# Kernel optimization log

Measured on AMD Instinct MI355X. Metric: run time of the kernel, lower is better.

## Reference

```python
import jax, jax.numpy as jnp
import numpy as np

N_DATA = 500000
EMB = 256
K = 4096
BS = 64
T = 0.07
M = 0.5


def _l2norm(x, axis=-1, eps=1e-12):
    return x / jnp.maximum(jnp.linalg.norm(x, axis=axis, keepdims=True), eps)


def setup_inputs() -> dict:
    key = jax.random.key(0)
    k1, k2, k3, k4, k5, k6 = jax.random.split(key, 6)
    vis_feat = jax.random.normal(k1, (BS, EMB), dtype=jnp.float32)
    text_feat = jax.random.normal(k2, (BS, EMB), dtype=jnp.float32)
    # memory banks: original inits uniform in [-stdv, stdv]; randn scaled works the same numerically
    stdv = 1.0 / np.sqrt(EMB / 3)
    vis_memory = jax.random.uniform(k3, (N_DATA, EMB), dtype=jnp.float32, minval=-stdv, maxval=stdv)
    text_memory = jax.random.uniform(k4, (N_DATA, EMB), dtype=jnp.float32, minval=-stdv, maxval=stdv)
    idx = jax.random.randint(k5, (BS,), 0, N_DATA, dtype=jnp.int32)
    slct_idx = jax.random.randint(k6, (BS, K + 1), 0, N_DATA, dtype=jnp.int32)
    # column 0 holds the positive index, as in slct_idx.select(1,0).copy_(idx)
    slct_idx = slct_idx.at[:, 0].set(idx)
    return {
        "vis_feat": vis_feat,
        "text_feat": text_feat,
        "vis_memory": vis_memory,
        "text_memory": text_memory,
        "slct_idx": slct_idx,
        "idx": idx,
    }


def reference(vis_feat, text_feat, vis_memory, text_memory, slct_idx, idx):
    # embeddings are L2-normalized before use (nn.functional.normalize(dim=1))
    vn = _l2norm(vis_feat)   # [bs, D]
    tn = _l2norm(text_feat)  # [bs, D]

    # gather K+1 negatives/positive from memory banks (detached in original)
    tf = jax.lax.stop_gradient(text_memory[slct_idx])  # [bs, K+1, D]
    vf = jax.lax.stop_gradient(vis_memory[slct_idx])   # [bs, K+1, D]

    # batched dot products + exp(./T) (bmm with [bs, D, 1])
    vis_out = jnp.exp(jnp.einsum("bkd,bd->bk", tf, vn) / T)   # [bs, K+1]
    text_out = jnp.exp(jnp.einsum("bkd,bd->bk", vf, tn) / T)  # [bs, K+1]

    # NCE normalization constants, set on first pass: Z = mean * N_data
    Z_v = jax.lax.stop_gradient(jnp.mean(vis_out)) * N_DATA
    Z_t = jax.lax.stop_gradient(jnp.mean(text_out)) * N_DATA
    vis_out = vis_out / Z_v
    text_out = text_out / Z_t

    # EMA memory update + renormalize + scatter (no_grad in original)
    vis_pos = vis_memory[idx] * M + jax.lax.stop_gradient(vn) * (1.0 - M)
    text_pos = text_memory[idx] * M + jax.lax.stop_gradient(tn) * (1.0 - M)
    new_vis_memory = vis_memory.at[idx].set(_l2norm(vis_pos))
    new_text_memory = text_memory.at[idx].set(_l2norm(text_pos))

    return vis_out, text_out, new_vis_memory, new_text_memory
```

## Files before the change

kernel.cpp:

```cpp
#include <hip/hip_runtime.h>

#define NDATA 500000
#define EMB   256
#define BS    64
#define KP1   4097
#define NPAIR (BS * KP1)
#define INV_T (1.0f / 0.07f)

#define SCAN_EPB 2048
#define NB_SCAN  ((NDATA + SCAN_EPB - 1) / SCAN_EPB)
#define RPW      32
#define NWAVES   (NDATA / RPW)
#define NBLKF    ((NWAVES + 3) / 4)
#define SSC_BLKS ((NPAIR + 255) / 256)
#define SCALE_BLKS ((2 * NPAIR + 255) / 256)
#define NBY      17

typedef float    f32x4 __attribute__((ext_vector_type(4)));
typedef unsigned u32x4 __attribute__((ext_vector_type(4)));

__global__ __launch_bounds__(256) void norm_hist_kernel(
    const float* __restrict__ vis_feat, const float* __restrict__ text_feat,
    float* __restrict__ vn, float* __restrict__ tn,
    const int* __restrict__ slct, unsigned* __restrict__ counts,
    unsigned* __restrict__ old) {
  int bid = blockIdx.x;
  if (bid < 128) {
    int b = bid & 63;
    bool is_vis = bid < 64;
    const float* src = (is_vis ? vis_feat : text_feat) + b * EMB;
    float* dst = (is_vis ? vn : tn) + b * EMB;
    int t = threadIdx.x;
    float x = src[t];
    float s = x * x;
    for (int off = 32; off > 0; off >>= 1) s += __shfl_down(s, off, 64);
    __shared__ float red[4];
    if ((t & 63) == 0) red[t >> 6] = s;
    __syncthreads();
    float norm = sqrtf(red[0] + red[1] + red[2] + red[3]);
    dst[t] = x / fmaxf(norm, 1e-12f);
  } else {
    int i = (bid - 128) * 256 + threadIdx.x;
    if (i < NPAIR) {
      int r = slct[i];
      old[i] = atomicAdd(&counts[r], 1u);
    }
  }
}

__global__ __launch_bounds__(256) void scan1_kernel(
    const unsigned* __restrict__ counts, unsigned* __restrict__ start,
    unsigned* __restrict__ bsum) {
  int t = threadIdx.x;
  int base = blockIdx.x * SCAN_EPB + t * 8;
  unsigned v[8];
  unsigned tsum = 0;
#pragma unroll
  for (int j = 0; j < 8; ++j) {
    int i = base + j;
    unsigned c = (i < NDATA) ? counts[i] : 0u;
    v[j] = tsum;
    tsum += c;
  }
  unsigned x = tsum;
  for (int d = 1; d < 64; d <<= 1) {
    unsigned y = __shfl_up(x, d, 64);
    if ((t & 63) >= d) x += y;
  }
  __shared__ unsigned wsum[4];
  if ((t & 63) == 63) wsum[t >> 6] = x;
  __syncthreads();
  unsigned woff = 0;
  for (int wv = 0; wv < (t >> 6); ++wv) woff += wsum[wv];
  unsigned ex = woff + x - tsum;
#pragma unroll
  for (int j = 0; j < 8; ++j) {
    int i = base + j;
    if (i < NDATA) start[i] = ex + v[j];
  }
  if (t == 255) bsum[blockIdx.x] = woff + x;
}

__global__ __launch_bounds__(256) void scan2_kernel(unsigned* __restrict__ bsum) {
  int t = threadIdx.x;
  unsigned v = (t < NB_SCAN) ? bsum[t] : 0u;
  unsigned x = v;
  for (int d = 1; d < 64; d <<= 1) {
    unsigned y = __shfl_up(x, d, 64);
    if ((t & 63) >= d) x += y;
  }
  __shared__ unsigned wsum[4];
  if ((t & 63) == 63) wsum[t >> 6] = x;
  __syncthreads();
  unsigned woff = 0;
  for (int wv = 0; wv < (t >> 6); ++wv) woff += wsum[wv];
  unsigned ex = woff + x - v;
  if (t < NB_SCAN) bsum[t] = ex;
}

__global__ __launch_bounds__(256) void scatter_kernel(
    const int* __restrict__ slct, const unsigned* __restrict__ start,
    const unsigned* __restrict__ bsum, const unsigned* __restrict__ old,
    unsigned* __restrict__ pairs) {
  int i = blockIdx.x * 256 + threadIdx.x;
  if (i < NPAIR) {
    int r = slct[i];
    unsigned pos = start[r] + bsum[r >> 11] + old[i];
    int b = i / KP1;
    int kk = i - b * KP1;
    pairs[pos] = ((unsigned)b << 13) | (unsigned)kk;
  }
}

#define LOADC(R, rb)                                                          \
  { _Pragma("unroll") for (int j = 0; j < 8; ++j)                             \
      R[j] = __builtin_nontemporal_load(&s4[(size_t)((rb) + j) * 64 + lane]); }

#define STOREC(R, rb)                                                         \
  { _Pragma("unroll") for (int j = 0; j < 8; ++j)                             \
      __builtin_nontemporal_store(R[j], &d4[(size_t)((rb) + j) * 64 + lane]); }

#define DOT4(Rj, fv) (Rj.x * fv.x + Rj.y * fv.y + Rj.z * fv.z + Rj.w * fv.w)

#define REFS(R, rb)                                                           \
  { u32x4 c0 = *(const u32x4*)&counts[(rb)];                                  \
    u32x4 c1 = *(const u32x4*)&counts[(rb) + 4];                              \
    u32x4 s0 = *(const u32x4*)&start[(rb)];                                   \
    u32x4 s1 = *(const u32x4*)&start[(rb) + 4];                               \
    unsigned cn[8] = {c0.x, c0.y, c0.z, c0.w, c1.x, c1.y, c1.z, c1.w};        \
    unsigned sn[8] = {s0.x, s0.y, s0.z, s0.w, s1.x, s1.y, s1.z, s1.w};        \
    _Pragma("unroll") for (int j = 0; j < 8; ++j) {                           \
      unsigned n = cn[j];                                                     \
      if (n) {                                                                \
        unsigned gs = sn[j] + bs;                                             \
        unsigned u = 0;                                                       \
        for (; u + 4 <= n; u += 4) {                                          \
          unsigned p0 = pairs[gs + u],     p1 = pairs[gs + u + 1];            \
          unsigned p2 = pairs[gs + u + 2], p3 = pairs[gs + u + 3];            \
          f32x4 f0 = f4[(p0 >> 13) * 64 + lane];                              \
          f32x4 f1 = f4[(p1 >> 13) * 64 + lane];                              \
          f32x4 f2 = f4[(p2 >> 13) * 64 + lane];                              \
          f32x4 f3 = f4[(p3 >> 13) * 64 + lane];                              \
          float d0 = DOT4(R[j], f0), d1 = DOT4(R[j], f1);                     \
          float d2 = DOT4(R[j], f2), d3 = DOT4(R[j], f3);                     \
          for (int off = 32; off > 0; off >>= 1) {                            \
            d0 += __shfl_down(d0, off, 64);                                   \
            d1 += __shfl_down(d1, off, 64);                                   \
            d2 += __shfl_down(d2, off, 64);                                   \
            d3 += __shfl_down(d3, off, 64);                                   \
          }                                                                   \
          if (lane == 0) {                                                    \
            float e0 = __expf(d0 * INV_T), e1 = __expf(d1 * INV_T);           \
            float e2 = __expf(d2 * INV_T), e3 = __expf(d3 * INV_T);           \
            tz[gs + u] = e0; tz[gs + u + 1] = e1;                             \
            tz[gs + u + 2] = e2; tz[gs + u + 3] = e3;                         \
            local += (e0 + e1) + (e2 + e3);                                   \
          }                                                                   \
        }                                                                     \
        for (; u < n; ++u) {                                                  \
          unsigned p = pairs[gs + u];                                         \
          f32x4 fv = f4[(p >> 13) * 64 + lane];                               \
          float d = DOT4(R[j], fv);                                           \
          for (int off = 32; off > 0; off >>= 1) d += __shfl_down(d, off, 64);\
          if (lane == 0) {                                                    \
            float e = __expf(d * INV_T);                                      \
            tz[gs + u] = e;                                                   \
            local += e;                                                       \
          }                                                                   \
        }                                                                     \
      }                                                                       \
    } }

__global__ __launch_bounds__(256) void fused_copy_dot_kernel(
    const float* __restrict__ text_mem, const float* __restrict__ vis_mem,
    float* __restrict__ out_text, float* __restrict__ out_vis,
    const float* __restrict__ vn, const float* __restrict__ tn,
    const unsigned* __restrict__ counts, const unsigned* __restrict__ start,
    const unsigned* __restrict__ bsum, const unsigned* __restrict__ pairs,
    float* __restrict__ tmp0, float* __restrict__ tmp1,
    float* __restrict__ zsum) {
  int z = blockIdx.z;
  const f32x4* s4 = (const f32x4*)(z == 0 ? text_mem : vis_mem);
  f32x4* d4 = (f32x4*)(z == 0 ? out_text : out_vis);
  const f32x4* f4 = (const f32x4*)(z == 0 ? vn : tn);
  float* tz = (z == 0) ? tmp0 : tmp1;

  int t = threadIdx.x, w = t >> 6, lane = t & 63;
  int gw = blockIdx.x * 4 + w;
  float local = 0.f;

  if (gw < NWAVES) {
    int r0 = gw * RPW;
    unsigned bs = bsum[r0 >> 11];
    f32x4 A[8], B[8];
    LOADC(A, r0);
    LOADC(B, r0 + 8);
    STOREC(A, r0);      REFS(A, r0);
    LOADC(A, r0 + 16);
    STOREC(B, r0 + 8);  REFS(B, r0 + 8);
    LOADC(B, r0 + 24);
    STOREC(A, r0 + 16); REFS(A, r0 + 16);
    STOREC(B, r0 + 24); REFS(B, r0 + 24);
  }
  __shared__ float red[4];
  if (lane == 0) red[w] = local;
  __syncthreads();
  if (t == 0) {
    float s = red[0] + red[1] + red[2] + red[3];
    atomicAdd(&zsum[z], s);
  }
}

__global__ __launch_bounds__(256) void scatter_scale_update_kernel(
    const unsigned* __restrict__ pairs,
    const float* __restrict__ tmp0, const float* __restrict__ tmp1,
    float* __restrict__ out, const float* __restrict__ zsum,
    const float* __restrict__ vis_mem, const float* __restrict__ text_mem,
    const float* __restrict__ vn, const float* __restrict__ tn,
    const int* __restrict__ idx,
    float* __restrict__ out_vis, float* __restrict__ out_text) {
  int bid = blockIdx.x;
  if (bid < SSC_BLKS) {
    int pos = bid * 256 + threadIdx.x;
    if (pos < NPAIR) {
      const float c = (float)NDATA / (float)NPAIR;
      unsigned p = pairs[pos];
      int o = (int)(p >> 13) * KP1 + (int)(p & 8191u);
      out[o]         = tmp0[pos] / (zsum[0] * c);
      out[NPAIR + o] = tmp1[pos] / (zsum[1] * c);
    }
  } else {
    int bb = bid - SSC_BLKS;
    int b = bb & 63;
    bool is_vis = bb < 64;
    int row = idx[b];
    for (int b2 = b + 1; b2 < BS; ++b2)
      if (idx[b2] == row) return;
    const float* mem  = (is_vis ? vis_mem : text_mem) + (size_t)row * EMB;
    const float* feat = (is_vis ? vn : tn) + b * EMB;
    float* dst = (is_vis ? out_vis : out_text) + (size_t)row * EMB;
    int t = threadIdx.x;
    float p = mem[t] * 0.5f + feat[t] * 0.5f;
    float s = p * p;
    for (int off = 32; off > 0; off >>= 1) s += __shfl_down(s, off, 64);
    __shared__ float red[4];
    if ((t & 63) == 0) red[t >> 6] = s;
    __syncthreads();
    float norm = sqrtf(red[0] + red[1] + red[2] + red[3]);
    dst[t] = p / fmaxf(norm, 1e-12f);
  }
}

__global__ __launch_bounds__(256) void dot_exp_kernel(
    const float* __restrict__ text_mem, const float* __restrict__ vis_mem,
    const float* __restrict__ vn, const float* __restrict__ tn,
    const int* __restrict__ slct, float* __restrict__ out,
    float* __restrict__ partials) {
  int b = blockIdx.x;
  int z = blockIdx.z;
  const float* mem  = (z == 0) ? text_mem : vis_mem;
  const float* feat = (z == 0) ? vn : tn;
  float* o = out + (size_t)z * NPAIR + (size_t)b * KP1;
  const int* srow = slct + b * KP1;
  __shared__ float4 sf[64];
  int t = threadIdx.x;
  if (t < 64) sf[t] = ((const float4*)(feat + b * EMB))[t];
  __syncthreads();
  int w = t >> 6, lane = t & 63;
  float4 f = sf[lane];
  int kbase = blockIdx.y * 256 + w * 64;
  int kend  = min(kbase + 64, KP1);
  float local = 0.f;
  int k = kbase;
  for (; k + 2 <= kend; k += 2) {
    int r0 = srow[k], r1 = srow[k + 1];
    float4 v0 = ((const float4*)(mem + (size_t)r0 * EMB))[lane];
    float4 v1 = ((const float4*)(mem + (size_t)r1 * EMB))[lane];
    float p0 = v0.x * f.x + v0.y * f.y + v0.z * f.z + v0.w * f.w;
    float p1 = v1.x * f.x + v1.y * f.y + v1.z * f.z + v1.w * f.w;
    for (int off = 32; off > 0; off >>= 1) {
      p0 += __shfl_down(p0, off, 64);
      p1 += __shfl_down(p1, off, 64);
    }
    if (lane == 0) {
      float e0 = __expf(p0 * INV_T);
      float e1 = __expf(p1 * INV_T);
      o[k] = e0; o[k + 1] = e1;
      local += e0 + e1;
    }
  }
  if (k < kend) {
    int r0 = srow[k];
    float4 v0 = ((const float4*)(mem + (size_t)r0 * EMB))[lane];
    float p0 = v0.x * f.x + v0.y * f.y + v0.z * f.z + v0.w * f.w;
    for (int off = 32; off > 0; off >>= 1) p0 += __shfl_down(p0, off, 64);
    if (lane == 0) { float e0 = __expf(p0 * INV_T); o[k] = e0; local += e0; }
  }
  __shared__ float red[4];
  if (lane == 0) red[w] = local;
  __syncthreads();
  if (t == 0)
    partials[((size_t)z * NBY + blockIdx.y) * BS + b] =
        red[0] + red[1] + red[2] + red[3];
}

__global__ __launch_bounds__(256) void reduce_z_kernel(
    const float* __restrict__ partials, float* __restrict__ zsum, int per_z) {
  int z = blockIdx.x;
  const float* p = partials + (size_t)z * per_z;
  float s = 0.f;
  for (int i = threadIdx.x; i < per_z; i += 256) s += p[i];
  for (int off = 32; off > 0; off >>= 1) s += __shfl_down(s, off, 64);
  __shared__ float red[4];
  if ((threadIdx.x & 63) == 0) red[threadIdx.x >> 6] = s;
  __syncthreads();
  if (threadIdx.x == 0) zsum[z] = red[0] + red[1] + red[2] + red[3];
}

__global__ __launch_bounds__(256) void copy2_kernel(
    const float4* __restrict__ src_a, float4* __restrict__ dst_a,
    const float4* __restrict__ src_b, float4* __restrict__ dst_b, long n4) {
  long i = (long)blockIdx.x * blockDim.x + threadIdx.x;
  long stride = (long)gridDim.x * blockDim.x;
  for (; i < 2 * n4; i += stride) {
    if (i < n4) dst_a[i] = src_a[i];
    else        dst_b[i - n4] = src_b[i - n4];
  }
}

__global__ __launch_bounds__(256) void scale_update_kernel(
    float* __restrict__ out, const float* __restrict__ zsum,
    const float* __restrict__ vis_mem, const float* __restrict__ text_mem,
    const float* __restrict__ vn, const float* __restrict__ tn,
    const int* __restrict__ idx,
    float* __restrict__ out_vis, float* __restrict__ out_text) {
  int bid = blockIdx.x;
  if (bid < SCALE_BLKS) {
    int i = bid * 256 + threadIdx.x;
    if (i < 2 * NPAIR) {
      float Z = ((i < NPAIR) ? zsum[0] : zsum[1]) * ((float)NDATA / (float)NPAIR);
      out[i] = out[i] / Z;
    }
  } else {
    int bb = bid - SCALE_BLKS;
    int b = bb & 63;
    bool is_vis = bb < 64;
    int row = idx[b];
    for (int b2 = b + 1; b2 < BS; ++b2)
      if (idx[b2] == row) return;
    const float* mem  = (is_vis ? vis_mem : text_mem) + (size_t)row * EMB;
    const float* feat = (is_vis ? vn : tn) + b * EMB;
    float* dst = (is_vis ? out_vis : out_text) + (size_t)row * EMB;
    int t = threadIdx.x;
    float p = mem[t] * 0.5f + feat[t] * 0.5f;
    float s = p * p;
    for (int off = 32; off > 0; off >>= 1) s += __shfl_down(s, off, 64);
    __shared__ float red[4];
    if ((t & 63) == 0) red[t >> 6] = s;
    __syncthreads();
    float norm = sqrtf(red[0] + red[1] + red[2] + red[3]);
    dst[t] = p / fmaxf(norm, 1e-12f);
  }
}

extern "C" void kernel_launch(void* const* d_in, const int* in_sizes, int n_in,
                              void* d_out, int out_size, void* d_ws, size_t ws_size,
                              hipStream_t stream) {
  const float* vis_feat  = (const float*)d_in[0];
  const float* text_feat = (const float*)d_in[1];
  const float* vis_mem   = (const float*)d_in[2];
  const float* text_mem  = (const float*)d_in[3];
  const int*   slct      = (const int*)d_in[4];
  const int*   idx       = (const int*)d_in[5];

  float* out          = (float*)d_out;
  float* out_vis_mem  = out + (size_t)2 * NPAIR;
  float* out_text_mem = out_vis_mem + (size_t)NDATA * EMB;

  float*    ws     = (float*)d_ws;
  float*    zsum   = ws;
  unsigned* counts = (unsigned*)(zsum + 4);
  unsigned* start  = counts + NDATA;
  unsigned* bsum   = start + NDATA;
  unsigned* old    = bsum + 256;
  unsigned* pairs  = old + NPAIR;
  float*    tmp1   = (float*)(pairs + NPAIR);
  float*    vn     = tmp1 + NPAIR;
  float*    tn     = vn + BS * EMB;
  float*    tmp0   = (float*)old;
  size_t needed = ((size_t)(4 + 2 * NDATA + 256 + 3 * NPAIR) +
                   (size_t)(2 * BS * EMB)) * 4;

  if (ws_size >= needed) {
    hipMemsetAsync(zsum, 0, (4 + NDATA) * sizeof(unsigned), stream);
    norm_hist_kernel<<<128 + (NPAIR + 255) / 256, 256, 0, stream>>>(
        vis_feat, text_feat, vn, tn, slct, counts, old);
    scan1_kernel<<<NB_SCAN, 256, 0, stream>>>(counts, start, bsum);
    scan2_kernel<<<1, 256, 0, stream>>>(bsum);
    scatter_kernel<<<(NPAIR + 255) / 256, 256, 0, stream>>>(slct, start, bsum, old, pairs);

    dim3 gF(NBLKF, 1, 2);
    fused_copy_dot_kernel<<<gF, 256, 0, stream>>>(
        text_mem, vis_mem, out_text_mem, out_vis_mem, vn, tn,
        counts, start, bsum, pairs, tmp0, tmp1, zsum);

    scatter_scale_update_kernel<<<SSC_BLKS + 128, 256, 0, stream>>>(
        pairs, tmp0, tmp1, out, zsum, vis_mem, text_mem, vn, tn, idx,
        out_vis_mem, out_text_mem);
  } else {
    norm_hist_kernel<<<128, 256, 0, stream>>>(
        vis_feat, text_feat, vn, tn, slct, counts, old);
    dim3 gB(BS, NBY, 2);
    dot_exp_kernel<<<gB, 256, 0, stream>>>(text_mem, vis_mem, vn, tn, slct, out,
                                           (float*)old);
    reduce_z_kernel<<<2, 256, 0, stream>>>((float*)old, zsum, NBY * BS);
    const long n4 = (long)NDATA * EMB / 4;
    copy2_kernel<<<8192, 256, 0, stream>>>(
        (const float4*)vis_mem,  (float4*)out_vis_mem,
        (const float4*)text_mem, (float4*)out_text_mem, n4);
    scale_update_kernel<<<SCALE_BLKS + 128, 256, 0, stream>>>(
        out, zsum, vis_mem, text_mem, vn, tn, idx, out_vis_mem, out_text_mem);
  }
}
```

Measured before the change: 421.3 us.

## Fuse block-sum scan into scatter kernel and interleave per-row reference loops

Merges the single-block scan2 kernel into the scatter kernel: every block recomputes the exclusive scan of block sums in shared memory, and block 0 writes the result to a separate bsum2 buffer. This removes one kernel launch and its dependency gap. It also rewrites the per-row reference processing in the fused copy/dot kernel so that the 8 rows of a chunk are handled together, iterating up to the maximum count and issuing up to 8 independent gathers and shuffle reductions per step. The aim is more memory-level parallelism in place of serial per-row loops, at the cost of predicated idle lanes when counts differ and more registers.

```diff
diff --git a/kernel.cpp b/kernel.cpp
--- a/kernel.cpp
+++ b/kernel.cpp
@@ -81,7 +81,12 @@
   if (t == 255) bsum[blockIdx.x] = woff + x;
 }
 
-__global__ __launch_bounds__(256) void scan2_kernel(unsigned* __restrict__ bsum) {
+__global__ __launch_bounds__(256) void scatter2_kernel(
+    const int* __restrict__ slct, const unsigned* __restrict__ start,
+    const unsigned* __restrict__ bsum, const unsigned* __restrict__ old,
+    unsigned* __restrict__ pairs, unsigned* __restrict__ bsum2) {
+  __shared__ unsigned sbs[256];
+  __shared__ unsigned wsum[4];
   int t = threadIdx.x;
   unsigned v = (t < NB_SCAN) ? bsum[t] : 0u;
   unsigned x = v;
@@ -89,23 +94,17 @@
     unsigned y = __shfl_up(x, d, 64);
     if ((t & 63) >= d) x += y;
   }
-  __shared__ unsigned wsum[4];
   if ((t & 63) == 63) wsum[t >> 6] = x;
   __syncthreads();
   unsigned woff = 0;
   for (int wv = 0; wv < (t >> 6); ++wv) woff += wsum[wv];
-  unsigned ex = woff + x - v;
-  if (t < NB_SCAN) bsum[t] = ex;
-}
-
-__global__ __launch_bounds__(256) void scatter_kernel(
-    const int* __restrict__ slct, const unsigned* __restrict__ start,
-    const unsigned* __restrict__ bsum, const unsigned* __restrict__ old,
-    unsigned* __restrict__ pairs) {
-  int i = blockIdx.x * 256 + threadIdx.x;
+  sbs[t] = woff + x - v;
+  __syncthreads();
+  if (blockIdx.x == 0) bsum2[t] = sbs[t];
+  int i = blockIdx.x * 256 + t;
   if (i < NPAIR) {
     int r = slct[i];
-    unsigned pos = start[r] + bsum[r >> 11] + old[i];
+    unsigned pos = start[r] + sbs[r >> 11] + old[i];
     int b = i / KP1;
     int kk = i - b * KP1;
     pairs[pos] = ((unsigned)b << 13) | (unsigned)kk;
@@ -122,61 +121,66 @@
 
 #define DOT4(Rj, fv) (Rj.x * fv.x + Rj.y * fv.y + Rj.z * fv.z + Rj.w * fv.w)
 
-#define REFS(R, rb)                                                           \
-  { u32x4 c0 = *(const u32x4*)&counts[(rb)];                                  \
-    u32x4 c1 = *(const u32x4*)&counts[(rb) + 4];                              \
-    u32x4 s0 = *(const u32x4*)&start[(rb)];                                   \
-    u32x4 s1 = *(const u32x4*)&start[(rb) + 4];                               \
-    unsigned cn[8] = {c0.x, c0.y, c0.z, c0.w, c1.x, c1.y, c1.z, c1.w};        \
-    unsigned sn[8] = {s0.x, s0.y, s0.z, s0.w, s1.x, s1.y, s1.z, s1.w};        \
-    _Pragma("unroll") for (int j = 0; j < 8; ++j) {                           \
-      unsigned n = cn[j];                                                     \
-      if (n) {                                                                \
-        unsigned gs = sn[j] + bs;                                             \
-        unsigned u = 0;                                                       \
-        for (; u + 4 <= n; u += 4) {                                          \
-          unsigned p0 = pairs[gs + u],     p1 = pairs[gs + u + 1];            \
-          unsigned p2 = pairs[gs + u + 2], p3 = pairs[gs + u + 3];            \
-          f32x4 f0 = f4[(p0 >> 13) * 64 + lane];                              \
-          f32x4 f1 = f4[(p1 >> 13) * 64 + lane];                              \
-          f32x4 f2 = f4[(p2 >> 13) * 64 + lane];                              \
-          f32x4 f3 = f4[(p3 >> 13) * 64 + lane];                              \
-          float d0 = DOT4(R[j], f0), d1 = DOT4(R[j], f1);                     \
-          float d2 = DOT4(R[j], f2), d3 = DOT4(R[j], f3);                     \
-          for (int off = 32; off > 0; off >>= 1) {                            \
-            d0 += __shfl_down(d0, off, 64);                                   \
-            d1 += __shfl_down(d1, off, 64);                                   \
-            d2 += __shfl_down(d2, off, 64);                                   \
-            d3 += __shfl_down(d3, off, 64);                                   \
-          }                                                                   \
-          if (lane == 0) {                                                    \
-            float e0 = __expf(d0 * INV_T), e1 = __expf(d1 * INV_T);           \
-            float e2 = __expf(d2 * INV_T), e3 = __expf(d3 * INV_T);           \
-            tz[gs + u] = e0; tz[gs + u + 1] = e1;                             \
-            tz[gs + u + 2] = e2; tz[gs + u + 3] = e3;                         \
-            local += (e0 + e1) + (e2 + e3);                                   \
-          }                                                                   \
-        }                                                                     \
-        for (; u < n; ++u) {                                                  \
-          unsigned p = pairs[gs + u];                                         \
-          f32x4 fv = f4[(p >> 13) * 64 + lane];                               \
-          float d = DOT4(R[j], fv);                                           \
-          for (int off = 32; off > 0; off >>= 1) d += __shfl_down(d, off, 64);\
-          if (lane == 0) {                                                    \
-            float e = __expf(d * INV_T);                                      \
-            tz[gs + u] = e;                                                   \
-            local += e;                                                       \
-          }                                                                   \
-        }                                                                     \
-      }                                                                       \
-    } }
+__device__ __forceinline__ void refs_chunk(
+    const f32x4* R, int rb, unsigned bso,
+    const unsigned* __restrict__ counts, const unsigned* __restrict__ start,
+    const unsigned* __restrict__ pairs, const f32x4* __restrict__ f4,
+    float* __restrict__ tz, int lane, float& local) {
+  u32x4 c0 = *(const u32x4*)&counts[rb];
+  u32x4 c1 = *(const u32x4*)&counts[rb + 4];
+  u32x4 s0 = *(const u32x4*)&start[rb];
+  u32x4 s1 = *(const u32x4*)&start[rb + 4];
+  unsigned cn[8] = {c0.x, c0.y, c0.z, c0.w, c1.x, c1.y, c1.z, c1.w};
+  unsigned sn[8] = {s0.x, s0.y, s0.z, s0.w, s1.x, s1.y, s1.z, s1.w};
+  unsigned gsb[8];
+  unsigned maxn = 0;
+#pragma unroll
+  for (int j = 0; j < 8; ++j) {
+    gsb[j] = sn[j] + bso;
+    maxn = maxn > cn[j] ? maxn : cn[j];
+  }
+  for (unsigned u = 0; u < maxn; ++u) {
+    unsigned pp[8];
+    f32x4 fv[8];
+    float d[8];
+#pragma unroll
+    for (int j = 0; j < 8; ++j)
+      if (cn[j] > u) pp[j] = pairs[gsb[j] + u];
+#pragma unroll
+    for (int j = 0; j < 8; ++j)
+      if (cn[j] > u) fv[j] = f4[(pp[j] >> 13) * 64 + lane];
+#pragma unroll
+    for (int j = 0; j < 8; ++j)
+      d[j] = (cn[j] > u) ? DOT4(R[j], fv[j]) : 0.f;
+#pragma unroll
+    for (int off = 32; off > 0; off >>= 1) {
+      d[0] += __shfl_down(d[0], off, 64);
+      d[1] += __shfl_down(d[1], off, 64);
+      d[2] += __shfl_down(d[2], off, 64);
+      d[3] += __shfl_down(d[3], off, 64);
+      d[4] += __shfl_down(d[4], off, 64);
+      d[5] += __shfl_down(d[5], off, 64);
+      d[6] += __shfl_down(d[6], off, 64);
+      d[7] += __shfl_down(d[7], off, 64);
+    }
+    if (lane == 0) {
+#pragma unroll
+      for (int j = 0; j < 8; ++j)
+        if (cn[j] > u) {
+          float e = __expf(d[j] * INV_T);
+          tz[gsb[j] + u] = e;
+          local += e;
+        }
+    }
+  }
+}
 
 __global__ __launch_bounds__(256) void fused_copy_dot_kernel(
     const float* __restrict__ text_mem, const float* __restrict__ vis_mem,
     float* __restrict__ out_text, float* __restrict__ out_vis,
     const float* __restrict__ vn, const float* __restrict__ tn,
     const unsigned* __restrict__ counts, const unsigned* __restrict__ start,
-    const unsigned* __restrict__ bsum, const unsigned* __restrict__ pairs,
+    const unsigned* __restrict__ bsum2, const unsigned* __restrict__ pairs,
     float* __restrict__ tmp0, float* __restrict__ tmp1,
     float* __restrict__ zsum) {
   int z = blockIdx.z;
@@ -191,16 +195,20 @@
 
   if (gw < NWAVES) {
     int r0 = gw * RPW;
-    unsigned bs = bsum[r0 >> 11];
+    unsigned bso = bsum2[r0 >> 11];
     f32x4 A[8], B[8];
     LOADC(A, r0);
     LOADC(B, r0 + 8);
-    STOREC(A, r0);      REFS(A, r0);
+    STOREC(A, r0);
+    refs_chunk(A, r0, bso, counts, start, pairs, f4, tz, lane, local);
     LOADC(A, r0 + 16);
-    STOREC(B, r0 + 8);  REFS(B, r0 + 8);
+    STOREC(B, r0 + 8);
+    refs_chunk(B, r0 + 8, bso, counts, start, pairs, f4, tz, lane, local);
     LOADC(B, r0 + 24);
-    STOREC(A, r0 + 16); REFS(A, r0 + 16);
-    STOREC(B, r0 + 24); REFS(B, r0 + 24);
+    STOREC(A, r0 + 16);
+    refs_chunk(A, r0 + 16, bso, counts, start, pairs, f4, tz, lane, local);
+    STOREC(B, r0 + 24);
+    refs_chunk(B, r0 + 24, bso, counts, start, pairs, f4, tz, lane, local);
   }
   __shared__ float red[4];
   if (lane == 0) red[w] = local;
@@ -382,13 +390,14 @@
   unsigned* counts = (unsigned*)(zsum + 4);
   unsigned* start  = counts + NDATA;
   unsigned* bsum   = start + NDATA;
-  unsigned* old    = bsum + 256;
+  unsigned* bsum2  = bsum + 256;
+  unsigned* old    = bsum2 + 256;
   unsigned* pairs  = old + NPAIR;
   float*    tmp1   = (float*)(pairs + NPAIR);
   float*    vn     = tmp1 + NPAIR;
   float*    tn     = vn + BS * EMB;
   float*    tmp0   = (float*)old;
-  size_t needed = ((size_t)(4 + 2 * NDATA + 256 + 3 * NPAIR) +
+  size_t needed = ((size_t)(4 + 2 * NDATA + 512 + 3 * NPAIR) +
                    (size_t)(2 * BS * EMB)) * 4;
 
   if (ws_size >= needed) {
@@ -396,13 +405,13 @@
     norm_hist_kernel<<<128 + (NPAIR + 255) / 256, 256, 0, stream>>>(
         vis_feat, text_feat, vn, tn, slct, counts, old);
     scan1_kernel<<<NB_SCAN, 256, 0, stream>>>(counts, start, bsum);
-    scan2_kernel<<<1, 256, 0, stream>>>(bsum);
-    scatter_kernel<<<(NPAIR + 255) / 256, 256, 0, stream>>>(slct, start, bsum, old, pairs);
+    scatter2_kernel<<<SSC_BLKS, 256, 0, stream>>>(slct, start, bsum, old, pairs,
+                                                  bsum2);
 
     dim3 gF(NBLKF, 1, 2);
     fused_copy_dot_kernel<<<gF, 256, 0, stream>>>(
         text_mem, vis_mem, out_text_mem, out_vis_mem, vn, tn,
-        counts, start, bsum, pairs, tmp0, tmp1, zsum);
+        counts, start, bsum2, pairs, tmp0, tmp1, zsum);
 
     scatter_scale_update_kernel<<<SSC_BLKS + 128, 256, 0, stream>>>(
         pairs, tmp0, tmp1, out, zsum, vis_mem, text_mem, vn, tn, idx,
```

Result: no change. 429.4 us (+1.9%).
